# Performance work log

Hardware: AMD Instinct MI355X
Metric: run time of the kernel (lower is better)

Reference implementation:

```python
import jax, jax.numpy as jnp
import numpy as np

N = 50000      # n_nodes == ninput
E = 800000     # edges
NHID = 96
N_INTER = 6
EPS = 1e-12


def _l2norm(x):
    # F.normalize(x, p=2, dim=1) with eps=1e-12
    n = jnp.linalg.norm(x, axis=1, keepdims=True)
    return x / jnp.maximum(n, EPS)


def _sage(x, src, dst, Wl, bl, Wr, n):
    # PyG SAGEConv (mean aggr): lin_l(mean_{j in N(i)} x_j) + lin_r(x_i)
    agg = jax.ops.segment_sum(x[src], dst, num_segments=n)          # [N, nhid]
    deg = jax.ops.segment_sum(jnp.ones((src.shape[0],), x.dtype), dst, num_segments=n)
    agg = agg / jnp.maximum(deg, 1.0)[:, None]
    return agg @ Wl + bl + x @ Wr


def _mlp(x, W1, b1, W2, b2, W3, b3):
    # GNN-Bet score MLP (eval mode, dropout p=0): nhid -> 2*nhid -> 2*nhid -> 1
    h = jax.nn.relu(x @ W1 + b1)
    h = jax.nn.relu(h @ W2 + b2)
    return h @ W3 + b3


def setup_inputs() -> dict:
    key = jax.random.key(0)
    ks = jax.random.split(key, 16)
    s = 0.05
    inp = {
        'edge_index1': jax.random.randint(ks[0], (2, E), 0, N, dtype=jnp.int32),
        'edge_vals1': jax.random.uniform(ks[1], (E,), dtype=jnp.float32),
        'edge_index2': jax.random.randint(ks[2], (2, E), 0, N, dtype=jnp.int32),
        # GNN_Layer_Init: weight [ninput=N, nhid], bias [nhid]
        'gc1_W': jax.random.normal(ks[3], (N, NHID), dtype=jnp.float32) * s,
        'gc1_b': jnp.zeros((NHID,), jnp.float32),
        # 7 SAGEConv layers (6 intermediate + gc_last), stacked
        'sage_Wl': jax.random.normal(ks[4], (7, NHID, NHID), dtype=jnp.float32) * s,
        'sage_bl': jnp.zeros((7, NHID), jnp.float32),
        'sage_Wr': jax.random.normal(ks[5], (7, NHID, NHID), dtype=jnp.float32) * s,
        # score MLP
        'mlp_W1': jax.random.normal(ks[6], (NHID, 2 * NHID), dtype=jnp.float32) * s,
        'mlp_b1': jnp.zeros((2 * NHID,), jnp.float32),
        'mlp_W2': jax.random.normal(ks[7], (2 * NHID, 2 * NHID), dtype=jnp.float32) * s,
        'mlp_b2': jnp.zeros((2 * NHID,), jnp.float32),
        'mlp_W3': jax.random.normal(ks[8], (2 * NHID, 1), dtype=jnp.float32) * s,
        'mlp_b3': jnp.zeros((1,), jnp.float32),
    }
    return inp


def reference(edge_index1, edge_vals1, edge_index2, gc1_W, gc1_b,
              sage_Wl, sage_bl, sage_Wr,
              mlp_W1, mlp_b1, mlp_W2, mlp_b2, mlp_W3, mlp_b3):
    # gc1: spmm(adj1, W) -> out[i] = sum_j adj1[i,j] * W[j]
    dst1, src1 = edge_index1[0], edge_index1[1]
    h0 = jax.ops.segment_sum(gc1_W[src1] * edge_vals1[:, None], dst1, num_segments=N) + gc1_b
    x2_1 = _l2norm(jax.nn.relu(h0))

    src2, dst2 = edge_index2[0], edge_index2[1]

    # main trunk: 6 intermediate SAGE layers applied sequentially
    x = x2_1
    for i in range(N_INTER):
        x = _l2norm(jax.nn.relu(_sage(x, src2, dst2, sage_Wl[i], sage_bl[i], sage_Wr[i], N)))
    x_last = jax.nn.relu(_sage(x, src2, dst2, sage_Wl[N_INTER], sage_bl[N_INTER], sage_Wr[N_INTER], N))

    # scores: MLP on x2_1, on each intermediate layer applied once to x2_1, and on x_last
    score = _mlp(x2_1, mlp_W1, mlp_b1, mlp_W2, mlp_b2, mlp_W3, mlp_b3)
    for i in range(N_INTER):
        xi = _l2norm(jax.nn.relu(_sage(x2_1, src2, dst2, sage_Wl[i], sage_bl[i], sage_Wr[i], N)))
        score = score + _mlp(xi, mlp_W1, mlp_b1, mlp_W2, mlp_b2, mlp_W3, mlp_b3)
    score = score + _mlp(x_last, mlp_W1, mlp_b1, mlp_W2, mlp_b2, mlp_W3, mlp_b3)
    return score  # [N, 1]
```

## Files before the change

### kernel.cpp

```cpp
#include <hip/hip_runtime.h>

#define NH 96
#define NH2 192

typedef __attribute__((ext_vector_type(8))) short short8;
typedef __attribute__((ext_vector_type(4))) float f32x4;

__device__ __forceinline__ unsigned short f2b(float f) {
  unsigned u = __float_as_uint(f);
  unsigned r = (u + 0x7FFFu + ((u >> 16) & 1u)) >> 16;
  return (unsigned short)r;
}
__device__ __forceinline__ float blo(unsigned w) { return __uint_as_float(w << 16); }
__device__ __forceinline__ float bhi(unsigned w) { return __uint_as_float(w & 0xFFFF0000u); }
__device__ __forceinline__ float b2f(short v) { return __uint_as_float(((unsigned)(unsigned short)v) << 16); }

__device__ __forceinline__ unsigned cvt_pk(float lo, float hi) {
  unsigned r;
  asm("v_cvt_pk_bf16_f32 %0, %1, %2" : "=v"(r) : "v"(lo), "v"(hi));
  return r;
}

__device__ __forceinline__ short8 u4_to_s8(int a, int b, int c, int d) {
  union { int u[4]; short8 s; } x;
  x.u[0] = a; x.u[1] = b; x.u[2] = c; x.u[3] = d;
  return x.s;
}

#define MFMA(a, b, c) __builtin_amdgcn_mfma_f32_16x16x32_bf16((a), (b), (c), 0, 0, 0)
#define WFRAG(p, idx) (*(const short8*)((p) + ((idx) << 9) + (l << 3)))

__device__ __forceinline__ void stage(unsigned short* dst, const unsigned short* src, int nshorts,
                                      int tid, int nt) {
  const uint4* s = (const uint4*)src;
  uint4* d = (uint4*)dst;
  int nv = nshorts >> 3;
  for (int i = tid; i < nv; i += nt) d[i] = s[i];
}

__device__ __forceinline__ short8 xchg(unsigned p0lo, unsigned p0hi, unsigned p1lo, unsigned p1hi,
                                       int srcA, int srcB, int hi) {
  int a0 = __shfl((int)p0lo, srcA), a1 = __shfl((int)p0hi, srcA);
  int c0 = __shfl((int)p1lo, srcA), c1 = __shfl((int)p1hi, srcA);
  int b0 = __shfl((int)p0lo, srcB), b1 = __shfl((int)p0hi, srcB);
  int d0 = __shfl((int)p1lo, srcB), d1 = __shfl((int)p1hi, srcB);
  return u4_to_s8(hi ? c0 : a0, hi ? c1 : a1, hi ? d0 : b0, hi ? d1 : b1);
}


__global__ void k_count(const int* __restrict__ dst1, const int* __restrict__ dst2,
                        int* __restrict__ cnt1, int* __restrict__ cnt2, int E, int psize, int cblocks,
                        const float* __restrict__ Wl, const float* __restrict__ Wr,
                        const float* __restrict__ W1, const float* __restrict__ W2,
                        const float* __restrict__ gW,
                        unsigned short* __restrict__ Wlp, unsigned short* __restrict__ Wrp,
                        unsigned short* __restrict__ W1p, unsigned short* __restrict__ W2p,
                        unsigned short* __restrict__ gwb, int gtotal) {
  if (blockIdx.x < (unsigned)cblocks) {
    int p = blockIdx.x & 7;
    int e = (blockIdx.x >> 3) * blockDim.x + threadIdx.x;
    if (e >= E) return;
    int lo = p * psize, hi = lo + psize;
    int d = dst1[e];
    if (d >= lo && d < hi) atomicAdd(&cnt1[d], 1);
    int dd = dst2[e];
    if (dd >= lo && dd < hi) atomicAdd(&cnt2[dd], 1);
    return;
  }
  int t = (blockIdx.x - cblocks) * blockDim.x + threadIdx.x;
  if (t < 129024) {
    bool isR = t >= 64512;
    int u = isR ? t - 64512 : t;
    int i = u / 9216, v = u % 9216;
    int tt = v / 1536, r = v % 1536;
    int kf = r / 512, w = r % 512, l = w >> 3, j = w & 7;
    int c = l & 15, g = l >> 4;
    int k = kf * 32 + g * 8 + j, nn = tt * 16 + c;
    float val = (isR ? Wr : Wl)[i * 9216 + k * 96 + nn];
    (isR ? Wrp : Wlp)[u] = f2b(val);
  } else if (t < 147456) {
    int u = t - 129024;
    int tt = u / 1536, r = u % 1536;
    int kf = r / 512, w = r % 512, l = w >> 3, j = w & 7;
    int c = l & 15, g = l >> 4;
    int k = kf * 32 + g * 8 + j, nn = tt * 16 + c;
    W1p[u] = f2b(W1[k * 192 + nn]);
  } else if (t < 184320) {
    int u = t - 147456;
    int tt = u / 3072, r = u % 3072;
    int kf = r / 512, w = r % 512, l = w >> 3, j = w & 7;
    int c = l & 15, g = l >> 4;
    int k = kf * 32 + g * 8 + j, nn = tt * 16 + c;
    W2p[u] = f2b(W2[k * 192 + nn]);
  } else {
    int i = (t - 184320) * 4;
    if (i + 3 < gtotal) {
      float4 v = *(const float4*)(gW + i);
      ushort4 o;
      o.x = f2b(v.x); o.y = f2b(v.y); o.z = f2b(v.z); o.w = f2b(v.w);
      *(ushort4*)(gwb + i) = o;
    }
  }
}


__global__ __launch_bounds__(256) void k_scanA(const int* __restrict__ cnt1, const int* __restrict__ cnt2,
                                               int* __restrict__ bs, int n) {
  int seg = blockIdx.y;
  const int* cnt = seg ? cnt2 : cnt1;
  int t = threadIdx.x;
  int idx = blockIdx.x * 1024 + t * 4;
  int sum = 0;
  if (idx + 3 < n) {
    int4 v = *(const int4*)(cnt + idx);
    sum = v.x + v.y + v.z + v.w;
  } else {
    for (int j = 0; j < 4; ++j) if (idx + j < n) sum += cnt[idx + j];
  }
  __shared__ int s[256];
  s[t] = sum;
  __syncthreads();
  for (int off = 128; off > 0; off >>= 1) {
    if (t < off) s[t] += s[t + off];
    __syncthreads();
  }
  if (t == 0) bs[seg * 64 + blockIdx.x] = s[0];
}

__global__ __launch_bounds__(128) void k_scanB(int* __restrict__ bs, int* __restrict__ rp1,
                                               int* __restrict__ rp2, int nb, int n) {
  int w = threadIdx.x >> 6, l = threadIdx.x & 63;
  int v = (l < nb) ? bs[w * 64 + l] : 0;
  int incl = v;
  for (int off = 1; off < 64; off <<= 1) {
    int u = __shfl_up(incl, off);
    if (l >= off) incl += u;
  }
  if (l < nb) bs[w * 64 + l] = incl - v;
  if (l == 63) {
    int* rp = w ? rp2 : rp1;
    rp[n] = incl;
  }
}

__global__ __launch_bounds__(256) void k_scanC(const int* __restrict__ cnt1, const int* __restrict__ cnt2,
                                               const int* __restrict__ bs,
                                               int* __restrict__ rp1, int* __restrict__ cur1,
                                               int* __restrict__ rp2, int* __restrict__ cur2, int n) {
  int seg = blockIdx.y;
  const int* cnt = seg ? cnt2 : cnt1;
  int* rp = seg ? rp2 : rp1;
  int* cur = seg ? cur2 : cur1;
  int t = threadIdx.x;
  int idx = blockIdx.x * 1024 + t * 4;
  int v[4] = {0, 0, 0, 0};
  if (idx + 3 < n) {
    int4 q = *(const int4*)(cnt + idx);
    v[0] = q.x; v[1] = q.y; v[2] = q.z; v[3] = q.w;
  } else {
    for (int j = 0; j < 4; ++j) if (idx + j < n) v[j] = cnt[idx + j];
  }
  int tsum = v[0] + v[1] + v[2] + v[3];
  __shared__ int s[256];
  s[t] = tsum;
  __syncthreads();
  for (int off = 1; off < 256; off <<= 1) {
    int u = (t >= off) ? s[t - off] : 0;
    __syncthreads();
    s[t] += u;
    __syncthreads();
  }
  int run = (t == 0 ? 0 : s[t - 1]) + bs[seg * 64 + blockIdx.x];
  for (int j = 0; j < 4; ++j) {
    if (idx + j < n) {
      rp[idx + j] = run;
      cur[idx + j] = run;
      run += v[j];
    }
  }
}

__global__ __launch_bounds__(1024) void k_scan(const int* __restrict__ cnt, int* __restrict__ rp,
                                               int* __restrict__ cur, int n) {
  __shared__ int s[1024];
  int tid = threadIdx.x;
  int chunk = (n + 1023) >> 10;
  int beg = tid * chunk;
  int end = min(beg + chunk, n);
  int sum = 0;
  for (int i = beg; i < end; ++i) sum += cnt[i];
  s[tid] = sum;
  __syncthreads();
  for (int off = 1; off < 1024; off <<= 1) {
    int v = (tid >= off) ? s[tid - off] : 0;
    __syncthreads();
    s[tid] += v;
    __syncthreads();
  }
  int excl = (tid == 0) ? 0 : s[tid - 1];
  for (int i = beg; i < end; ++i) { rp[i] = excl; cur[i] = excl; excl += cnt[i]; }
  if (tid == 1023) rp[n] = s[1023];
}

__global__ void k_scatter(const int* __restrict__ d1, const int* __restrict__ s1, const float* __restrict__ v1,
                          int* __restrict__ cur1, int2* __restrict__ c1sv,
                          const int* __restrict__ s2, const int* __restrict__ d2,
                          int* __restrict__ cur2, int* __restrict__ c2s, int E, int psize) {
  int p = blockIdx.x & 7;
  int e = (blockIdx.x >> 3) * blockDim.x + threadIdx.x;
  if (e >= E) return;
  int lo = p * psize, hi = lo + psize;
  int d = d1[e];
  if (d >= lo && d < hi) {
    int pos = atomicAdd(&cur1[d], 1);
    c1sv[pos] = make_int2(s1[e], __float_as_int(v1[e]));
  }
  int dd = d2[e];
  if (dd >= lo && dd < hi) {
    int pos = atomicAdd(&cur2[dd], 1);
    c2s[pos] = s2[e];
  }
}


__global__ __launch_bounds__(256) void k_gc1(const int* __restrict__ rp, const int2* __restrict__ cv,
                                             const unsigned short* __restrict__ Wb,
                                             const float* __restrict__ b, unsigned short* __restrict__ out, int n) {
  int gw = (blockIdx.x * 256 + threadIdx.x) >> 6;
  int l = threadIdx.x & 63;
  if (gw >= n) return;
  int s = rp[gw], e = rp[gw + 1];
  bool act = l < 48;
  float a0 = 0.f, a1 = 0.f, b0 = 0.f, b1 = 0.f, c0 = 0.f, c1 = 0.f, d0 = 0.f, d1 = 0.f;
  int i = s;
  for (; i + 3 < e; i += 4) {
    int2 q0 = cv[i], q1 = cv[i + 1], q2 = cv[i + 2], q3 = cv[i + 3];
    if (act) {
      unsigned w0 = *(const unsigned*)(Wb + (size_t)q0.x * NH + 2 * l);
      unsigned w1 = *(const unsigned*)(Wb + (size_t)q1.x * NH + 2 * l);
      unsigned w2 = *(const unsigned*)(Wb + (size_t)q2.x * NH + 2 * l);
      unsigned w3 = *(const unsigned*)(Wb + (size_t)q3.x * NH + 2 * l);
      float v0 = __int_as_float(q0.y), v1 = __int_as_float(q1.y);
      float v2 = __int_as_float(q2.y), v3 = __int_as_float(q3.y);
      a0 = fmaf(v0, blo(w0), a0); a1 = fmaf(v0, bhi(w0), a1);
      b0 = fmaf(v1, blo(w1), b0); b1 = fmaf(v1, bhi(w1), b1);
      c0 = fmaf(v2, blo(w2), c0); c1 = fmaf(v2, bhi(w2), c1);
      d0 = fmaf(v3, blo(w3), d0); d1 = fmaf(v3, bhi(w3), d1);
    }
  }
  for (; i < e; ++i) {
    int2 q0 = cv[i];
    if (act) {
      unsigned w0 = *(const unsigned*)(Wb + (size_t)q0.x * NH + 2 * l);
      float v0 = __int_as_float(q0.y);
      a0 = fmaf(v0, blo(w0), a0); a1 = fmaf(v0, bhi(w0), a1);
    }
  }
  a0 += b0 + c0 + d0; a1 += b1 + c1 + d1;
  if (act) {
    a0 = fmaxf(a0 + b[2 * l], 0.f);
    a1 = fmaxf(a1 + b[2 * l + 1], 0.f);
  } else { a0 = a1 = 0.f; }
  float ss = a0 * a0 + a1 * a1;
#pragma unroll
  for (int o = 1; o < 64; o <<= 1) ss += __shfl_xor(ss, o);
  float sc = 1.f / fmaxf(sqrtf(ss), 1e-12f);
  if (act) {
    unsigned pk = ((unsigned)f2b(a1 * sc) << 16) | f2b(a0 * sc);
    ((unsigned*)out)[(size_t)gw * 48 + l] = pk;
  }
}


__global__ __launch_bounds__(256) void k_agg(const int* __restrict__ rp, const int* __restrict__ csrc,
                                             const unsigned short* __restrict__ X,
                                             unsigned short* __restrict__ out, int n) {
  int gw = (blockIdx.x * 256 + threadIdx.x) >> 6;
  int l = threadIdx.x & 63;
  if (gw >= n) return;
  int s = rp[gw], e = rp[gw + 1];
  bool act = l < 48;
  float a0 = 0.f, a1 = 0.f, b0 = 0.f, b1 = 0.f, c0 = 0.f, c1 = 0.f, d0 = 0.f, d1 = 0.f;
  int i = s;
  for (; i + 3 < e; i += 4) {
    int s0 = csrc[i], s1 = csrc[i + 1], s2 = csrc[i + 2], s3 = csrc[i + 3];
    if (act) {
      unsigned w0 = *(const unsigned*)(X + (size_t)s0 * NH + 2 * l);
      unsigned w1 = *(const unsigned*)(X + (size_t)s1 * NH + 2 * l);
      unsigned w2 = *(const unsigned*)(X + (size_t)s2 * NH + 2 * l);
      unsigned w3 = *(const unsigned*)(X + (size_t)s3 * NH + 2 * l);
      a0 += blo(w0); a1 += bhi(w0);
      b0 += blo(w1); b1 += bhi(w1);
      c0 += blo(w2); c1 += bhi(w2);
      d0 += blo(w3); d1 += bhi(w3);
    }
  }
  for (; i < e; ++i) {
    int s0 = csrc[i];
    if (act) {
      unsigned w0 = *(const unsigned*)(X + (size_t)s0 * NH + 2 * l);
      a0 += blo(w0); a1 += bhi(w0);
    }
  }
  a0 += b0 + c0 + d0; a1 += b1 + c1 + d1;
  float inv = 1.f / fmaxf((float)(e - s), 1.f);
  if (act) {
    unsigned pk = ((unsigned)f2b(a1 * inv) << 16) | f2b(a0 * inv);
    ((unsigned*)out)[(size_t)gw * 48 + l] = pk;
  }
}


template <int EPI>
__device__ __forceinline__ void sage_body(int blk, int nwaves, unsigned short* sw,
                                          const int* __restrict__ rp, const int* __restrict__ csrc,
                                          const unsigned short* __restrict__ X,
                                          const unsigned short* __restrict__ Wlp,
                                          const unsigned short* __restrict__ Wrp,
                                          const float* __restrict__ bias,
                                          unsigned short* __restrict__ Y, int n) {
  int tid = threadIdx.x;
  int l = tid & 63;
  int m0 = (blk * nwaves + (tid >> 6)) * 16;
  int c = l & 15, g = l >> 4;

  stage(sw, Wlp, 9216, tid, nwaves * 64);
  stage(sw + 9216, Wrp, 9216, tid, nwaves * 64);
  __syncthreads();

  int nd = min(m0 + c, n - 1);
  int s = rp[nd], e = rp[nd + 1];

  float aa[3][8], bb[3][8];
#pragma unroll
  for (int kf = 0; kf < 3; ++kf)
#pragma unroll
    for (int j = 0; j < 8; ++j) { aa[kf][j] = 0.f; bb[kf][j] = 0.f; }

  const unsigned short* Xg = X + g * 8;
  int i = s;
  for (; i + 1 < e; i += 2) {
    const unsigned short* xr0 = Xg + (size_t)csrc[i] * NH;
    const unsigned short* xr1 = Xg + (size_t)csrc[i + 1] * NH;
    short8 a0 = *(const short8*)(xr0);
    short8 a1 = *(const short8*)(xr0 + 32);
    short8 a2 = *(const short8*)(xr0 + 64);
    short8 b0 = *(const short8*)(xr1);
    short8 b1 = *(const short8*)(xr1 + 32);
    short8 b2 = *(const short8*)(xr1 + 64);
#pragma unroll
    for (int j = 0; j < 8; ++j) {
      aa[0][j] += b2f(a0[j]); aa[1][j] += b2f(a1[j]); aa[2][j] += b2f(a2[j]);
      bb[0][j] += b2f(b0[j]); bb[1][j] += b2f(b1[j]); bb[2][j] += b2f(b2[j]);
    }
  }
  if (i < e) {
    const unsigned short* xr0 = Xg + (size_t)csrc[i] * NH;
    short8 a0 = *(const short8*)(xr0);
    short8 a1 = *(const short8*)(xr0 + 32);
    short8 a2 = *(const short8*)(xr0 + 64);
#pragma unroll
    for (int j = 0; j < 8; ++j) {
      aa[0][j] += b2f(a0[j]); aa[1][j] += b2f(a1[j]); aa[2][j] += b2f(a2[j]);
    }
  }
  float inv = 1.f / fmaxf((float)(e - s), 1.f);
  short8 af[3];
#pragma unroll
  for (int kf = 0; kf < 3; ++kf)
#pragma unroll
    for (int j = 0; j < 8; ++j) af[kf][j] = (short)f2b((aa[kf][j] + bb[kf][j]) * inv);

  size_t aoff = (size_t)nd * NH + g * 8;
  short8 xf[3];
#pragma unroll
  for (int kf = 0; kf < 3; ++kf) xf[kf] = *(const short8*)(X + aoff + kf * 32);

  f32x4 acc[6];
#pragma unroll
  for (int t = 0; t < 6; ++t) acc[t] = (f32x4){0.f, 0.f, 0.f, 0.f};
#pragma unroll
  for (int kf = 0; kf < 3; ++kf) {
#pragma unroll
    for (int t = 0; t < 6; ++t) {
      short8 wlf = WFRAG(sw, t * 3 + kf);
      acc[t] = MFMA(wlf, af[kf], acc[t]);
    }
#pragma unroll
    for (int t = 0; t < 6; ++t) {
      short8 wrf = WFRAG(sw + 9216, t * 3 + kf);
      acc[t] = MFMA(wrf, xf[kf], acc[t]);
    }
  }

  float v[6][4];
  float ss = 0.f;
#pragma unroll
  for (int t = 0; t < 6; ++t) {
    float4 bv = *(const float4*)(bias + t * 16 + g * 4);
#pragma unroll
    for (int r = 0; r < 4; ++r) {
      float x = fmaxf(acc[t][r] + ((const float*)&bv)[r], 0.f);
      v[t][r] = x;
      ss = fmaf(x, x, ss);
    }
  }
  if (EPI == 0) {
    ss += __shfl_xor(ss, 16);
    ss += __shfl_xor(ss, 32);
    float sc = 1.f / fmaxf(sqrtf(ss), 1e-12f);
#pragma unroll
    for (int t = 0; t < 6; ++t)
#pragma unroll
      for (int r = 0; r < 4; ++r) v[t][r] *= sc;
  }
  if (m0 + c < n) {
    unsigned short* yr = Y + (size_t)(m0 + c) * NH;
#pragma unroll
    for (int t = 0; t < 6; ++t)
      *(uint2*)(yr + t * 16 + g * 4) = make_uint2(cvt_pk(v[t][0], v[t][1]), cvt_pk(v[t][2], v[t][3]));
  }
}

template <int EPI>
__global__ __launch_bounds__(256) void k_sageagg(const int* __restrict__ rp, const int* __restrict__ csrc,
                                                 const unsigned short* __restrict__ X,
                                                 const unsigned short* __restrict__ Wlp,
                                                 const unsigned short* __restrict__ Wrp,
                                                 const float* __restrict__ bias,
                                                 unsigned short* __restrict__ Y, int n) {
  __shared__ __align__(16) unsigned short sw[18432];
  sage_body<EPI>(blockIdx.x, 4, sw, rp, csrc, X, Wlp, Wrp, bias, Y, n);
}


__global__ __launch_bounds__(256) void k_mlp(const unsigned short* __restrict__ X,
                                             const unsigned short* __restrict__ W1p, const float* __restrict__ b1,
                                             const unsigned short* __restrict__ W2p, const float* __restrict__ b2,
                                             const float* __restrict__ W3, const float* __restrict__ b3,
                                             float* __restrict__ score, int n) {
  __shared__ __align__(16) unsigned short sw[18432];
  int tid = threadIdx.x;
  int l = tid & 63;
  int m0 = (blockIdx.x * 4 + (tid >> 6)) * 32;
  int c = l & 15, g = l >> 4;
  int srcA = c + ((g & 1) << 5), srcB = srcA + 16, hi = g >> 1;
  int rA = min(m0 + c, n - 1), rB = min(m0 + 16 + c, n - 1);

  stage(sw, W1p, 18432, tid, 256);

  short8 xf[2][3];
#pragma unroll
  for (int kf = 0; kf < 3; ++kf) {
    xf[0][kf] = *(const short8*)(X + (size_t)rA * NH + kf * 32 + g * 8);
    xf[1][kf] = *(const short8*)(X + (size_t)rB * NH + kf * 32 + g * 8);
  }
  __syncthreads();

  unsigned pk1[2][12][2];
#pragma unroll
  for (int t = 0; t < 12; ++t) {
    f32x4 a0 = (f32x4){0.f, 0.f, 0.f, 0.f};
    f32x4 a1 = (f32x4){0.f, 0.f, 0.f, 0.f};
#pragma unroll
    for (int kf = 0; kf < 3; ++kf) {
      short8 wf = WFRAG(sw, t * 3 + kf);
      a0 = MFMA(wf, xf[0][kf], a0);
      a1 = MFMA(wf, xf[1][kf], a1);
    }
    float4 bv = *(const float4*)(b1 + t * 16 + g * 4);
    pk1[0][t][0] = cvt_pk(fmaxf(a0[0] + bv.x, 0.f), fmaxf(a0[1] + bv.y, 0.f));
    pk1[0][t][1] = cvt_pk(fmaxf(a0[2] + bv.z, 0.f), fmaxf(a0[3] + bv.w, 0.f));
    pk1[1][t][0] = cvt_pk(fmaxf(a1[0] + bv.x, 0.f), fmaxf(a1[1] + bv.y, 0.f));
    pk1[1][t][1] = cvt_pk(fmaxf(a1[2] + bv.z, 0.f), fmaxf(a1[3] + bv.w, 0.f));
  }

  short8 af2[2][6];
#pragma unroll
  for (int kf = 0; kf < 6; ++kf) {
    af2[0][kf] = xchg(pk1[0][2 * kf][0], pk1[0][2 * kf][1], pk1[0][2 * kf + 1][0], pk1[0][2 * kf + 1][1], srcA, srcB, hi);
    af2[1][kf] = xchg(pk1[1][2 * kf][0], pk1[1][2 * kf][1], pk1[1][2 * kf + 1][0], pk1[1][2 * kf + 1][1], srcA, srcB, hi);
  }

  float sv0 = 0.f, sv1 = 0.f;
#pragma unroll
  for (int h = 0; h < 2; ++h) {
    __syncthreads();
    stage(sw, W2p + h * 18432, 18432, tid, 256);
    __syncthreads();
#pragma unroll
    for (int tt = 0; tt < 6; ++tt) {
      int t = h * 6 + tt;
      f32x4 a0 = (f32x4){0.f, 0.f, 0.f, 0.f};
      f32x4 a1 = (f32x4){0.f, 0.f, 0.f, 0.f};
#pragma unroll
      for (int kf = 0; kf < 6; ++kf) {
        short8 wf = WFRAG(sw, tt * 6 + kf);
        a0 = MFMA(wf, af2[0][kf], a0);
        a1 = MFMA(wf, af2[1][kf], a1);
      }
      float4 bv = *(const float4*)(b2 + t * 16 + g * 4);
      float4 wv3 = *(const float4*)(W3 + t * 16 + g * 4);
#pragma unroll
      for (int r = 0; r < 4; ++r) {
        sv0 = fmaf(fmaxf(a0[r] + ((const float*)&bv)[r], 0.f), ((const float*)&wv3)[r], sv0);
        sv1 = fmaf(fmaxf(a1[r] + ((const float*)&bv)[r], 0.f), ((const float*)&wv3)[r], sv1);
      }
    }
  }
  sv0 += __shfl_xor(sv0, 16); sv0 += __shfl_xor(sv0, 32);
  sv1 += __shfl_xor(sv1, 16); sv1 += __shfl_xor(sv1, 32);
  if (g == 0) {
    float b3v = b3[0];
    if (m0 + c < n) score[m0 + c] += sv0 + b3v;
    if (m0 + 16 + c < n) score[m0 + 16 + c] += sv1 + b3v;
  }
}


__device__ __forceinline__ void branch_body(int bb, int blk, unsigned short* sw,
                                            const unsigned short* __restrict__ Ag,
                                            const unsigned short* __restrict__ X21,
                                            const unsigned short* __restrict__ Wlp,
                                            const unsigned short* __restrict__ Wrp,
                                            const float* __restrict__ sbl,
                                            const unsigned short* __restrict__ W1p, const float* __restrict__ b1,
                                            const unsigned short* __restrict__ W2p, const float* __restrict__ b2,
                                            const float* __restrict__ W3, const float* __restrict__ b3,
                                            unsigned short* __restrict__ Xb, float* __restrict__ score, int n) {
  int tid = threadIdx.x;
  int l = tid & 63;
  int m0 = (blk * 8 + (tid >> 6)) * 32;
  int c = l & 15, g = l >> 4;
  int srcA = c + ((g & 1) << 5), srcB = srcA + 16, hi = g >> 1;
  int rA = min(m0 + c, n - 1), rB = min(m0 + 16 + c, n - 1);
  size_t aoffA = (size_t)rA * NH + g * 8, aoffB = (size_t)rB * NH + g * 8;

  short8 af1[2][3];

  if (bb < 6) {
    const float* bl = sbl + (size_t)bb * NH;
    stage(sw, Wlp + (size_t)bb * 9216, 9216, tid, 512);
    stage(sw + 9216, Wrp + (size_t)bb * 9216, 9216, tid, 512);

    short8 agf[2][3], xf[2][3];
#pragma unroll
    for (int kf = 0; kf < 3; ++kf) {
      agf[0][kf] = *(const short8*)(Ag + aoffA + kf * 32);
      agf[1][kf] = *(const short8*)(Ag + aoffB + kf * 32);
      xf[0][kf] = *(const short8*)(X21 + aoffA + kf * 32);
      xf[1][kf] = *(const short8*)(X21 + aoffB + kf * 32);
    }
    __syncthreads();

    float v[2][6][4];
    float ss0 = 0.f, ss1 = 0.f;
#pragma unroll
    for (int t = 0; t < 6; ++t) {
      f32x4 a0 = (f32x4){0.f, 0.f, 0.f, 0.f};
      f32x4 a1 = (f32x4){0.f, 0.f, 0.f, 0.f};
#pragma unroll
      for (int kf = 0; kf < 3; ++kf) {
        short8 wlf = WFRAG(sw, t * 3 + kf);
        a0 = MFMA(wlf, agf[0][kf], a0);
        a1 = MFMA(wlf, agf[1][kf], a1);
        short8 wrf = WFRAG(sw + 9216, t * 3 + kf);
        a0 = MFMA(wrf, xf[0][kf], a0);
        a1 = MFMA(wrf, xf[1][kf], a1);
      }
      float4 bv = *(const float4*)(bl + t * 16 + g * 4);
#pragma unroll
      for (int r = 0; r < 4; ++r) {
        float x0 = fmaxf(a0[r] + ((const float*)&bv)[r], 0.f);
        float x1 = fmaxf(a1[r] + ((const float*)&bv)[r], 0.f);
        v[0][t][r] = x0; ss0 = fmaf(x0, x0, ss0);
        v[1][t][r] = x1; ss1 = fmaf(x1, x1, ss1);
      }
    }
    ss0 += __shfl_xor(ss0, 16); ss0 += __shfl_xor(ss0, 32);
    ss1 += __shfl_xor(ss1, 16); ss1 += __shfl_xor(ss1, 32);
    float sc0 = 1.f / fmaxf(sqrtf(ss0), 1e-12f);
    float sc1 = 1.f / fmaxf(sqrtf(ss1), 1e-12f);

    unsigned pk[2][6][2];
#pragma unroll
    for (int t = 0; t < 6; ++t) {
      pk[0][t][0] = cvt_pk(v[0][t][0] * sc0, v[0][t][1] * sc0);
      pk[0][t][1] = cvt_pk(v[0][t][2] * sc0, v[0][t][3] * sc0);
      pk[1][t][0] = cvt_pk(v[1][t][0] * sc1, v[1][t][1] * sc1);
      pk[1][t][1] = cvt_pk(v[1][t][2] * sc1, v[1][t][3] * sc1);
    }
    if (bb == 0) {
      if (m0 + c < n) {
        unsigned short* yr = Xb + (size_t)(m0 + c) * NH;
#pragma unroll
        for (int t = 0; t < 6; ++t) *(uint2*)(yr + t * 16 + g * 4) = make_uint2(pk[0][t][0], pk[0][t][1]);
      }
      if (m0 + 16 + c < n) {
        unsigned short* yr = Xb + (size_t)(m0 + 16 + c) * NH;
#pragma unroll
        for (int t = 0; t < 6; ++t) *(uint2*)(yr + t * 16 + g * 4) = make_uint2(pk[1][t][0], pk[1][t][1]);
      }
    }

    __syncthreads();
    stage(sw, W1p, 18432, tid, 512);
#pragma unroll
    for (int kf = 0; kf < 3; ++kf) {
      af1[0][kf] = xchg(pk[0][2 * kf][0], pk[0][2 * kf][1], pk[0][2 * kf + 1][0], pk[0][2 * kf + 1][1], srcA, srcB, hi);
      af1[1][kf] = xchg(pk[1][2 * kf][0], pk[1][2 * kf][1], pk[1][2 * kf + 1][0], pk[1][2 * kf + 1][1], srcA, srcB, hi);
    }
    __syncthreads();
  } else {
#pragma unroll
    for (int kf = 0; kf < 3; ++kf) {
      af1[0][kf] = *(const short8*)(X21 + aoffA + kf * 32);
      af1[1][kf] = *(const short8*)(X21 + aoffB + kf * 32);
    }
    stage(sw, W1p, 18432, tid, 512);
    __syncthreads();
  }

  unsigned pk1[2][12][2];
#pragma unroll
  for (int t = 0; t < 12; ++t) {
    f32x4 a0 = (f32x4){0.f, 0.f, 0.f, 0.f};
    f32x4 a1 = (f32x4){0.f, 0.f, 0.f, 0.f};
#pragma unroll
    for (int kf = 0; kf < 3; ++kf) {
      short8 wf = WFRAG(sw, t * 3 + kf);
      a0 = MFMA(wf, af1[0][kf], a0);
      a1 = MFMA(wf, af1[1][kf], a1);
    }
    float4 bv = *(const float4*)(b1 + t * 16 + g * 4);
    pk1[0][t][0] = cvt_pk(fmaxf(a0[0] + bv.x, 0.f), fmaxf(a0[1] + bv.y, 0.f));
    pk1[0][t][1] = cvt_pk(fmaxf(a0[2] + bv.z, 0.f), fmaxf(a0[3] + bv.w, 0.f));
    pk1[1][t][0] = cvt_pk(fmaxf(a1[0] + bv.x, 0.f), fmaxf(a1[1] + bv.y, 0.f));
    pk1[1][t][1] = cvt_pk(fmaxf(a1[2] + bv.z, 0.f), fmaxf(a1[3] + bv.w, 0.f));
  }

  short8 af2[2][6];
#pragma unroll
  for (int kf = 0; kf < 6; ++kf) {
    af2[0][kf] = xchg(pk1[0][2 * kf][0], pk1[0][2 * kf][1], pk1[0][2 * kf + 1][0], pk1[0][2 * kf + 1][1], srcA, srcB, hi);
    af2[1][kf] = xchg(pk1[1][2 * kf][0], pk1[1][2 * kf][1], pk1[1][2 * kf + 1][0], pk1[1][2 * kf + 1][1], srcA, srcB, hi);
  }
  float sv0 = 0.f, sv1 = 0.f;
#pragma unroll
  for (int h = 0; h < 2; ++h) {
    __syncthreads();
    stage(sw, W2p + h * 18432, 18432, tid, 512);
    __syncthreads();
#pragma unroll
    for (int tt = 0; tt < 6; ++tt) {
      int t = h * 6 + tt;
      f32x4 a0 = (f32x4){0.f, 0.f, 0.f, 0.f};
      f32x4 a1 = (f32x4){0.f, 0.f, 0.f, 0.f};
#pragma unroll
      for (int kf = 0; kf < 6; ++kf) {
        short8 wf = WFRAG(sw, tt * 6 + kf);
        a0 = MFMA(wf, af2[0][kf], a0);
        a1 = MFMA(wf, af2[1][kf], a1);
      }
      float4 bv = *(const float4*)(b2 + t * 16 + g * 4);
      float4 wv3 = *(const float4*)(W3 + t * 16 + g * 4);
#pragma unroll
      for (int r = 0; r < 4; ++r) {
        sv0 = fmaf(fmaxf(a0[r] + ((const float*)&bv)[r], 0.f), ((const float*)&wv3)[r], sv0);
        sv1 = fmaf(fmaxf(a1[r] + ((const float*)&bv)[r], 0.f), ((const float*)&wv3)[r], sv1);
      }
    }
  }
  sv0 += __shfl_xor(sv0, 16); sv0 += __shfl_xor(sv0, 32);
  sv1 += __shfl_xor(sv1, 16); sv1 += __shfl_xor(sv1, 32);
  if (g == 0) {
    float b3v = b3[0];
    if (m0 + c < n) atomicAdd(&score[m0 + c], sv0 + b3v);
    if (m0 + 16 + c < n) atomicAdd(&score[m0 + 16 + c], sv1 + b3v);
  }
}

__global__ __launch_bounds__(512) void k_branchA(const unsigned short* __restrict__ Ag,
                                                 const unsigned short* __restrict__ X21,
                                                 const unsigned short* __restrict__ Wlp,
                                                 const unsigned short* __restrict__ Wrp,
                                                 const float* __restrict__ sbl,
                                                 const unsigned short* __restrict__ W1p, const float* __restrict__ b1,
                                                 const unsigned short* __restrict__ W2p, const float* __restrict__ b2,
                                                 const float* __restrict__ W3, const float* __restrict__ b3,
                                                 unsigned short* __restrict__ Xb, float* __restrict__ score,
                                                 int n, int nblk) {
  __shared__ __align__(16) unsigned short sw[18432];
  int bb = (blockIdx.x >= (unsigned)nblk) ? 6 : 0;
  int blk = blockIdx.x - (bb ? nblk : 0);
  branch_body(bb, blk, sw, Ag, X21, Wlp, Wrp, sbl, W1p, b1, W2p, b2, W3, b3, Xb, score, n);
}

__global__ __launch_bounds__(512) void k_mega(const unsigned short* __restrict__ Ag,
                                              const unsigned short* __restrict__ X21,
                                              const unsigned short* __restrict__ Wlp,
                                              const unsigned short* __restrict__ Wrp,
                                              const float* __restrict__ sbl,
                                              const unsigned short* __restrict__ W1p, const float* __restrict__ b1,
                                              const unsigned short* __restrict__ W2p, const float* __restrict__ b2,
                                              const float* __restrict__ W3, const float* __restrict__ b3,
                                              float* __restrict__ score,
                                              const int* __restrict__ rp2, const int* __restrict__ c2s,
                                              const unsigned short* __restrict__ Xb, unsigned short* __restrict__ Tb,
                                              int n, int nblk, int nbranch) {
  __shared__ __align__(16) unsigned short sw[18432];
  if (blockIdx.x < (unsigned)nbranch) {
    int bb = 1 + blockIdx.x / nblk;
    int blk = blockIdx.x - (bb - 1) * nblk;
    branch_body(bb, blk, sw, Ag, X21, Wlp, Wrp, sbl, W1p, b1, W2p, b2, W3, b3, nullptr, score, n);
  } else {
    sage_body<0>(blockIdx.x - nbranch, 8, sw, rp2, c2s, Xb,
                 Wlp + 9216, Wrp + 9216, sbl + NH, Tb, n);
  }
}


extern "C" void kernel_launch(void* const* d_in, const int* in_sizes, int n_in,
                              void* d_out, int out_size, void* d_ws, size_t ws_size,
                              hipStream_t stream) {
  const int* ei1 = (const int*)d_in[0];
  const float* ev1 = (const float*)d_in[1];
  const int* ei2 = (const int*)d_in[2];
  const float* gW = (const float*)d_in[3];
  const float* gb = (const float*)d_in[4];
  const float* sWl = (const float*)d_in[5];
  const float* sbl = (const float*)d_in[6];
  const float* sWr = (const float*)d_in[7];
  const float* W1 = (const float*)d_in[8];
  const float* b1 = (const float*)d_in[9];
  const float* W2 = (const float*)d_in[10];
  const float* b2 = (const float*)d_in[11];
  const float* W3 = (const float*)d_in[12];
  const float* b3 = (const float*)d_in[13];
  float* score = (float*)d_out;

  const int E = in_sizes[0] / 2;
  const int n = in_sizes[3] / NH;

  const int* d1 = ei1;
  const int* s1 = ei1 + E;
  const int* s2 = ei2;
  const int* d2 = ei2 + E;

  char* w = (char*)d_ws;
  auto alloc = [&](size_t bytes) {
    char* p = w;
    w += (bytes + 255) & ~(size_t)255;
    return p;
  };
  int* cnt1 = (int*)alloc((size_t)n * 4);
  int* cnt2 = (int*)alloc((size_t)n * 4);
  int* cur1 = (int*)alloc((size_t)n * 4);
  int* cur2 = (int*)alloc((size_t)n * 4);
  int* rp1 = (int*)alloc((size_t)(n + 1) * 4);
  int* rp2 = (int*)alloc((size_t)(n + 1) * 4);
  int* bs = (int*)alloc(128 * 4);
  int2* c1sv = (int2*)alloc((size_t)E * 8);
  int* c2s = (int*)alloc((size_t)E * 4);
  unsigned short* gwb = (unsigned short*)alloc((size_t)n * NH * 2);
  unsigned short* wlp = (unsigned short*)alloc((size_t)7 * NH * NH * 2);
  unsigned short* wrp = (unsigned short*)alloc((size_t)7 * NH * NH * 2);
  unsigned short* w1p = (unsigned short*)alloc((size_t)NH * NH2 * 2);
  unsigned short* w2p = (unsigned short*)alloc((size_t)NH2 * NH2 * 2);
  unsigned short* x21 = (unsigned short*)alloc((size_t)n * NH * 2);
  unsigned short* Ag = (unsigned short*)alloc((size_t)n * NH * 2);
  unsigned short* xb = (unsigned short*)alloc((size_t)n * NH * 2);
  unsigned short* tb = (unsigned short*)alloc((size_t)n * NH * 2);

  size_t zbytes = (size_t)((char*)cur1 - (char*)cnt1) + (size_t)n * 4;
  hipMemsetAsync(cnt1, 0, zbytes, stream);
  hipMemsetAsync(score, 0, (size_t)n * 4, stream);

  int eb = (E + 255) / 256;
  int nb4 = (n + 3) / 4;
  int sblk = (n + 63) / 64;
  int gblk = (n + 127) / 128;
  int nblk = (n + 255) / 256;
  int tblk8 = (n + 127) / 128;
  int psize = (n + 7) / 8;
  int nb1024 = (n + 1023) / 1024;
  int gtotal = n * NH;
  int prep_blocks = (184320 + gtotal / 4 + 255) / 256;

  k_count<<<eb * 8 + prep_blocks, 256, 0, stream>>>(d1, d2, cnt1, cnt2, E, psize, eb * 8,
                                                    sWl, sWr, W1, W2, gW, wlp, wrp, w1p, w2p, gwb, gtotal);
  if (nb1024 <= 64) {
    k_scanA<<<dim3(nb1024, 2), 256, 0, stream>>>(cnt1, cnt2, bs, n);
    k_scanB<<<1, 128, 0, stream>>>(bs, rp1, rp2, nb1024, n);
    k_scanC<<<dim3(nb1024, 2), 256, 0, stream>>>(cnt1, cnt2, bs, rp1, cur1, rp2, cur2, n);
  } else {
    k_scan<<<1, 1024, 0, stream>>>(cnt1, rp1, cur1, n);
    k_scan<<<1, 1024, 0, stream>>>(cnt2, rp2, cur2, n);
  }
  k_scatter<<<eb * 8, 256, 0, stream>>>(d1, s1, ev1, cur1, c1sv, s2, d2, cur2, c2s, E, psize);

  k_gc1<<<nb4, 256, 0, stream>>>(rp1, c1sv, gwb, gb, x21, n);

  k_agg<<<nb4, 256, 0, stream>>>(rp2, c2s, x21, Ag, n);

  k_branchA<<<2 * nblk, 512, 0, stream>>>(Ag, x21, wlp, wrp, sbl, w1p, b1, w2p, b2, W3, b3,
                                          xb, score, n, nblk);

  k_mega<<<5 * nblk + tblk8, 512, 0, stream>>>(Ag, x21, wlp, wrp, sbl, w1p, b1, w2p, b2, W3, b3,
                                               score, rp2, c2s, xb, tb, n, nblk, 5 * nblk);

  unsigned short* xc = tb;
  unsigned short* xn = xb;
  for (int i = 2; i < 6; ++i) {
    k_sageagg<0><<<sblk, 256, 0, stream>>>(rp2, c2s, xc, wlp + (size_t)i * 9216,
                                           wrp + (size_t)i * 9216, sbl + (size_t)i * NH, xn, n);
    unsigned short* tmp = xc; xc = xn; xn = tmp;
  }

  k_sageagg<1><<<sblk, 256, 0, stream>>>(rp2, c2s, xc, wlp + (size_t)6 * 9216,
                                         wrp + (size_t)6 * 9216, sbl + (size_t)6 * NH, xn, n);
  k_mlp<<<gblk, 256, 0, stream>>>(xn, w1p, b1, w2p, b2, W3, b3, score, n);

  (void)n_in; (void)out_size; (void)ws_size;
}
```

Before: 554.1 us.

## Fuse last SAGE layer with score MLP and unroll neighbor gather by four

The final SAGE layer (gc_last) is merged with the score MLP into one kernel, k_last. The relu'd layer output stays in registers and is remapped into MFMA operand layout with lane shuffles, so it is never written to or reloaded from global memory and one launch is removed. The neighbor mean-gather is moved into a shared helper and unrolled to four rows per iteration, giving more memory loads in flight. In exchange, the MLP stage now handles 16 rows per wave instead of 32, so MLP weight staging per row doubles, and register pressure rises.

```diff
diff --git a/kernel.cpp b/kernel.cpp
--- a/kernel.cpp
+++ b/kernel.cpp
@@ -45,6 +45,52 @@
   int b0 = __shfl((int)p0lo, srcB), b1 = __shfl((int)p0hi, srcB);
   int d0 = __shfl((int)p1lo, srcB), d1 = __shfl((int)p1hi, srcB);
   return u4_to_s8(hi ? c0 : a0, hi ? c1 : a1, hi ? d0 : b0, hi ? d1 : b1);
+}
+
+__device__ __forceinline__ void gather_mean(const int* __restrict__ rp, const int* __restrict__ csrc,
+                                            const unsigned short* __restrict__ X,
+                                            int nd, int g, short8 af[3]) {
+  int s = rp[nd], e = rp[nd + 1];
+  float aa[3][8], bb[3][8];
+#pragma unroll
+  for (int kf = 0; kf < 3; ++kf)
+#pragma unroll
+    for (int j = 0; j < 8; ++j) { aa[kf][j] = 0.f; bb[kf][j] = 0.f; }
+
+  const unsigned short* Xg = X + g * 8;
+  int i = s;
+  for (; i + 3 < e; i += 4) {
+    const unsigned short* x0 = Xg + (size_t)csrc[i] * NH;
+    const unsigned short* x1 = Xg + (size_t)csrc[i + 1] * NH;
+    const unsigned short* x2 = Xg + (size_t)csrc[i + 2] * NH;
+    const unsigned short* x3 = Xg + (size_t)csrc[i + 3] * NH;
+    short8 r00 = *(const short8*)(x0), r01 = *(const short8*)(x0 + 32), r02 = *(const short8*)(x0 + 64);
+    short8 r10 = *(const short8*)(x1), r11 = *(const short8*)(x1 + 32), r12 = *(const short8*)(x1 + 64);
+    short8 r20 = *(const short8*)(x2), r21 = *(const short8*)(x2 + 32), r22 = *(const short8*)(x2 + 64);
+    short8 r30 = *(const short8*)(x3), r31 = *(const short8*)(x3 + 32), r32 = *(const short8*)(x3 + 64);
+#pragma unroll
+    for (int j = 0; j < 8; ++j) {
+      aa[0][j] += b2f(r00[j]) + b2f(r20[j]);
+      aa[1][j] += b2f(r01[j]) + b2f(r21[j]);
+      aa[2][j] += b2f(r02[j]) + b2f(r22[j]);
+      bb[0][j] += b2f(r10[j]) + b2f(r30[j]);
+      bb[1][j] += b2f(r11[j]) + b2f(r31[j]);
+      bb[2][j] += b2f(r12[j]) + b2f(r32[j]);
+    }
+  }
+  for (; i < e; ++i) {
+    const unsigned short* x0 = Xg + (size_t)csrc[i] * NH;
+    short8 r0 = *(const short8*)(x0), r1 = *(const short8*)(x0 + 32), r2 = *(const short8*)(x0 + 64);
+#pragma unroll
+    for (int j = 0; j < 8; ++j) {
+      aa[0][j] += b2f(r0[j]); aa[1][j] += b2f(r1[j]); aa[2][j] += b2f(r2[j]);
+    }
+  }
+  float inv = 1.f / fmaxf((float)(e - s), 1.f);
+#pragma unroll
+  for (int kf = 0; kf < 3; ++kf)
+#pragma unroll
+    for (int j = 0; j < 8; ++j) af[kf][j] = (short)f2b((aa[kf][j] + bb[kf][j]) * inv);
 }
 
 
@@ -329,47 +375,8 @@
   __syncthreads();
 
   int nd = min(m0 + c, n - 1);
-  int s = rp[nd], e = rp[nd + 1];
-
-  float aa[3][8], bb[3][8];
-#pragma unroll
-  for (int kf = 0; kf < 3; ++kf)
-#pragma unroll
-    for (int j = 0; j < 8; ++j) { aa[kf][j] = 0.f; bb[kf][j] = 0.f; }
-
-  const unsigned short* Xg = X + g * 8;
-  int i = s;
-  for (; i + 1 < e; i += 2) {
-    const unsigned short* xr0 = Xg + (size_t)csrc[i] * NH;
-    const unsigned short* xr1 = Xg + (size_t)csrc[i + 1] * NH;
-    short8 a0 = *(const short8*)(xr0);
-    short8 a1 = *(const short8*)(xr0 + 32);
-    short8 a2 = *(const short8*)(xr0 + 64);
-    short8 b0 = *(const short8*)(xr1);
-    short8 b1 = *(const short8*)(xr1 + 32);
-    short8 b2 = *(const short8*)(xr1 + 64);
-#pragma unroll
-    for (int j = 0; j < 8; ++j) {
-      aa[0][j] += b2f(a0[j]); aa[1][j] += b2f(a1[j]); aa[2][j] += b2f(a2[j]);
-      bb[0][j] += b2f(b0[j]); bb[1][j] += b2f(b1[j]); bb[2][j] += b2f(b2[j]);
-    }
-  }
-  if (i < e) {
-    const unsigned short* xr0 = Xg + (size_t)csrc[i] * NH;
-    short8 a0 = *(const short8*)(xr0);
-    short8 a1 = *(const short8*)(xr0 + 32);
-    short8 a2 = *(const short8*)(xr0 + 64);
-#pragma unroll
-    for (int j = 0; j < 8; ++j) {
-      aa[0][j] += b2f(a0[j]); aa[1][j] += b2f(a1[j]); aa[2][j] += b2f(a2[j]);
-    }
-  }
-  float inv = 1.f / fmaxf((float)(e - s), 1.f);
   short8 af[3];
-#pragma unroll
-  for (int kf = 0; kf < 3; ++kf)
-#pragma unroll
-    for (int j = 0; j < 8; ++j) af[kf][j] = (short)f2b((aa[kf][j] + bb[kf][j]) * inv);
+  gather_mean(rp, csrc, X, nd, g, af);
 
   size_t aoff = (size_t)nd * NH + g * 8;
   short8 xf[3];
@@ -434,55 +441,92 @@
 }
 
 
-__global__ __launch_bounds__(256) void k_mlp(const unsigned short* __restrict__ X,
-                                             const unsigned short* __restrict__ W1p, const float* __restrict__ b1,
-                                             const unsigned short* __restrict__ W2p, const float* __restrict__ b2,
-                                             const float* __restrict__ W3, const float* __restrict__ b3,
-                                             float* __restrict__ score, int n) {
+__global__ __launch_bounds__(256) void k_last(const int* __restrict__ rp, const int* __restrict__ csrc,
+                                              const unsigned short* __restrict__ X,
+                                              const unsigned short* __restrict__ Wlp,
+                                              const unsigned short* __restrict__ Wrp,
+                                              const float* __restrict__ bias,
+                                              const unsigned short* __restrict__ W1p, const float* __restrict__ b1,
+                                              const unsigned short* __restrict__ W2p, const float* __restrict__ b2,
+                                              const float* __restrict__ W3, const float* __restrict__ b3,
+                                              float* __restrict__ score, int n) {
   __shared__ __align__(16) unsigned short sw[18432];
   int tid = threadIdx.x;
   int l = tid & 63;
-  int m0 = (blockIdx.x * 4 + (tid >> 6)) * 32;
+  int m0 = (blockIdx.x * 4 + (tid >> 6)) * 16;
   int c = l & 15, g = l >> 4;
   int srcA = c + ((g & 1) << 5), srcB = srcA + 16, hi = g >> 1;
-  int rA = min(m0 + c, n - 1), rB = min(m0 + 16 + c, n - 1);
-
+
+  stage(sw, Wlp, 9216, tid, 256);
+  stage(sw + 9216, Wrp, 9216, tid, 256);
+  __syncthreads();
+
+  int nd = min(m0 + c, n - 1);
+  short8 af[3];
+  gather_mean(rp, csrc, X, nd, g, af);
+
+  size_t aoff = (size_t)nd * NH + g * 8;
+  short8 xf[3];
+#pragma unroll
+  for (int kf = 0; kf < 3; ++kf) xf[kf] = *(const short8*)(X + aoff + kf * 32);
+
+  f32x4 acc[6];
+#pragma unroll
+  for (int t = 0; t < 6; ++t) acc[t] = (f32x4){0.f, 0.f, 0.f, 0.f};
+#pragma unroll
+  for (int kf = 0; kf < 3; ++kf) {
+#pragma unroll
+    for (int t = 0; t < 6; ++t) {
+      short8 wlf = WFRAG(sw, t * 3 + kf);
+      acc[t] = MFMA(wlf, af[kf], acc[t]);
+    }
+#pragma unroll
+    for (int t = 0; t < 6; ++t) {
+      short8 wrf = WFRAG(sw + 9216, t * 3 + kf);
+      acc[t] = MFMA(wrf, xf[kf], acc[t]);
+    }
+  }
+
+  unsigned pk[6][2];
+#pragma unroll
+  for (int t = 0; t < 6; ++t) {
+    float4 bv = *(const float4*)(bias + t * 16 + g * 4);
+    float x0 = fmaxf(acc[t][0] + bv.x, 0.f);
+    float x1 = fmaxf(acc[t][1] + bv.y, 0.f);
+    float x2 = fmaxf(acc[t][2] + bv.z, 0.f);
+    float x3 = fmaxf(acc[t][3] + bv.w, 0.f);
+    pk[t][0] = cvt_pk(x0, x1);
+    pk[t][1] = cvt_pk(x2, x3);
+  }
+
+  __syncthreads();
   stage(sw, W1p, 18432, tid, 256);
-
-  short8 xf[2][3];
-#pragma unroll
-  for (int kf = 0; kf < 3; ++kf) {
-    xf[0][kf] = *(const short8*)(X + (size_t)rA * NH + kf * 32 + g * 8);
-    xf[1][kf] = *(const short8*)(X + (size_t)rB * NH + kf * 32 + g * 8);
-  }
+  short8 af1[3];
+#pragma unroll
+  for (int kf = 0; kf < 3; ++kf)
+    af1[kf] = xchg(pk[2 * kf][0], pk[2 * kf][1], pk[2 * kf + 1][0], pk[2 * kf + 1][1], srcA, srcB, hi);
   __syncthreads();
 
-  unsigned pk1[2][12][2];
+  unsigned pk1[12][2];
 #pragma unroll
   for (int t = 0; t < 12; ++t) {
     f32x4 a0 = (f32x4){0.f, 0.f, 0.f, 0.f};
-    f32x4 a1 = (f32x4){0.f, 0.f, 0.f, 0.f};
 #pragma unroll
     for (int kf = 0; kf < 3; ++kf) {
       short8 wf = WFRAG(sw, t * 3 + kf);
-      a0 = MFMA(wf, xf[0][kf], a0);
-      a1 = MFMA(wf, xf[1][kf], a1);
+      a0 = MFMA(wf, af1[kf], a0);
     }
     float4 bv = *(const float4*)(b1 + t * 16 + g * 4);
-    pk1[0][t][0] = cvt_pk(fmaxf(a0[0] + bv.x, 0.f), fmaxf(a0[1] + bv.y, 0.f));
-    pk1[0][t][1] = cvt_pk(fmaxf(a0[2] + bv.z, 0.f), fmaxf(a0[3] + bv.w, 0.f));
-    pk1[1][t][0] = cvt_pk(fmaxf(a1[0] + bv.x, 0.f), fmaxf(a1[1] + bv.y, 0.f));
-    pk1[1][t][1] = cvt_pk(fmaxf(a1[2] + bv.z, 0.f), fmaxf(a1[3] + bv.w, 0.f));
-  }
-
-  short8 af2[2][6];
-#pragma unroll
-  for (int kf = 0; kf < 6; ++kf) {
-    af2[0][kf] = xchg(pk1[0][2 * kf][0], pk1[0][2 * kf][1], pk1[0][2 * kf + 1][0], pk1[0][2 * kf + 1][1], srcA, srcB, hi);
-    af2[1][kf] = xchg(pk1[1][2 * kf][0], pk1[1][2 * kf][1], pk1[1][2 * kf + 1][0], pk1[1][2 * kf + 1][1], srcA, srcB, hi);
-  }
-
-  float sv0 = 0.f, sv1 = 0.f;
+    pk1[t][0] = cvt_pk(fmaxf(a0[0] + bv.x, 0.f), fmaxf(a0[1] + bv.y, 0.f));
+    pk1[t][1] = cvt_pk(fmaxf(a0[2] + bv.z, 0.f), fmaxf(a0[3] + bv.w, 0.f));
+  }
+
+  short8 af2[6];
+#pragma unroll
+  for (int kf = 0; kf < 6; ++kf)
+    af2[kf] = xchg(pk1[2 * kf][0], pk1[2 * kf][1], pk1[2 * kf + 1][0], pk1[2 * kf + 1][1], srcA, srcB, hi);
+
+  float sv = 0.f;
 #pragma unroll
   for (int h = 0; h < 2; ++h) {
     __syncthreads();
@@ -492,29 +536,21 @@
     for (int tt = 0; tt < 6; ++tt) {
       int t = h * 6 + tt;
       f32x4 a0 = (f32x4){0.f, 0.f, 0.f, 0.f};
-      f32x4 a1 = (f32x4){0.f, 0.f, 0.f, 0.f};
 #pragma unroll
       for (int kf = 0; kf < 6; ++kf) {
         short8 wf = WFRAG(sw, tt * 6 + kf);
-        a0 = MFMA(wf, af2[0][kf], a0);
-        a1 = MFMA(wf, af2[1][kf], a1);
+        a0 = MFMA(wf, af2[kf], a0);
       }
       float4 bv = *(const float4*)(b2 + t * 16 + g * 4);
       float4 wv3 = *(const float4*)(W3 + t * 16 + g * 4);
 #pragma unroll
-      for (int r = 0; r < 4; ++r) {
-        sv0 = fmaf(fmaxf(a0[r] + ((const float*)&bv)[r], 0.f), ((const float*)&wv3)[r], sv0);
-        sv1 = fmaf(fmaxf(a1[r] + ((const float*)&bv)[r], 0.f), ((const float*)&wv3)[r], sv1);
-      }
-    }
-  }
-  sv0 += __shfl_xor(sv0, 16); sv0 += __shfl_xor(sv0, 32);
-  sv1 += __shfl_xor(sv1, 16); sv1 += __shfl_xor(sv1, 32);
-  if (g == 0) {
-    float b3v = b3[0];
-    if (m0 + c < n) score[m0 + c] += sv0 + b3v;
-    if (m0 + 16 + c < n) score[m0 + 16 + c] += sv1 + b3v;
-  }
+      for (int r = 0; r < 4; ++r)
+        sv = fmaf(fmaxf(a0[r] + ((const float*)&bv)[r], 0.f), ((const float*)&wv3)[r], sv);
+    }
+  }
+  sv += __shfl_xor(sv, 16);
+  sv += __shfl_xor(sv, 32);
+  if (g == 0 && m0 + c < n) score[m0 + c] += sv + b3[0];
 }
 
 
@@ -779,7 +815,6 @@
   int eb = (E + 255) / 256;
   int nb4 = (n + 3) / 4;
   int sblk = (n + 63) / 64;
-  int gblk = (n + 127) / 128;
   int nblk = (n + 255) / 256;
   int tblk8 = (n + 127) / 128;
   int psize = (n + 7) / 8;
@@ -817,9 +852,8 @@
     unsigned short* tmp = xc; xc = xn; xn = tmp;
   }
 
-  k_sageagg<1><<<sblk, 256, 0, stream>>>(rp2, c2s, xc, wlp + (size_t)6 * 9216,
-                                         wrp + (size_t)6 * 9216, sbl + (size_t)6 * NH, xn, n);
-  k_mlp<<<gblk, 256, 0, stream>>>(xn, w1p, b1, w2p, b2, W3, b3, score, n);
+  k_last<<<sblk, 256, 0, stream>>>(rp2, c2s, xc, wlp + (size_t)6 * 9216, wrp + (size_t)6 * 9216,
+                                   sbl + (size_t)6 * NH, w1p, b1, w2p, b2, W3, b3, score, n);
 
   (void)n_in; (void)out_size; (void)ws_size;
 }
```

Measured after the change: 575.4 us. +3.8%, slower.
